# Kernel tuning notes

Hardware: AMD Instinct MI355X
Metric: run time of the kernel (lower is better)

## Reference

```python
import jax, jax.numpy as jnp
import numpy as np

D_IN = 1024
D_OUT = 1024

def setup_inputs() -> dict:
    key = jax.random.key(0)
    ks = jax.random.split(key, 7)
    s = 1.0 / np.sqrt(D_IN)
    x = jax.random.normal(ks[0], (4, 2048, D_IN), dtype=jnp.float32)
    Wq = jax.random.uniform(ks[1], (D_IN, D_OUT), jnp.float32, -s, s)
    Wk = jax.random.uniform(ks[2], (D_IN, D_OUT), jnp.float32, -s, s)
    Wv = jax.random.uniform(ks[3], (D_IN, D_OUT), jnp.float32, -s, s)
    bq = jax.random.uniform(ks[4], (D_OUT,), jnp.float32, -s, s)
    bk = jax.random.uniform(ks[5], (D_OUT,), jnp.float32, -s, s)
    bv = jax.random.uniform(ks[6], (D_OUT,), jnp.float32, -s, s)
    return {"x": x, "Wq": Wq, "Wk": Wk, "Wv": Wv, "bq": bq, "bk": bk, "bv": bv}

def reference(x, Wq, Wk, Wv, bq, bk, bv):
    # x: [b, n, d_in]
    q = jnp.einsum('bnd,de->bne', x, Wq) + bq
    k = jnp.einsum('bnd,de->bne', x, Wk) + bk
    v = jnp.einsum('bnd,de->bne', x, Wv) + bv
    scale = 1.0 / jnp.sqrt(jnp.asarray(k.shape[-1], dtype=x.dtype))
    scores = jnp.einsum('bqe,bke->bqk', q, k) * scale  # [b, n, n]
    weights = jax.nn.softmax(scores, axis=-1)
    return jnp.einsum('bqk,bke->bqe', weights, v)
```

## Files before the change

### kernel.cpp

```cpp
#include <hip/hip_runtime.h>
#include <cstdint>

typedef __bf16 bf16x8 __attribute__((ext_vector_type(8)));
typedef float f32x16 __attribute__((ext_vector_type(16)));

__device__ __forceinline__ unsigned short f2b(float f) {
    union { float f; uint32_t u; } x; x.f = f;
    uint32_t r = (x.u + 0x7fffu + ((x.u >> 16) & 1u)) >> 16;
    return (unsigned short)r;
}
__device__ __forceinline__ float b2f(unsigned short h) {
    union { float f; uint32_t u; } x; x.u = ((uint32_t)h) << 16;
    return x.f;
}

__global__ __launch_bounds__(256) void convert_x_kernel(const float* __restrict__ x,
                                                        unsigned short* __restrict__ xb) {
    int i = (blockIdx.x * 256 + threadIdx.x) * 4;
    float4 v = *(const float4*)(x + i);
    ushort4 o;
    o.x = f2b(v.x); o.y = f2b(v.y); o.z = f2b(v.z); o.w = f2b(v.w);
    *(ushort4*)(xb + i) = o;
}

__global__ __launch_bounds__(1024) void transpose_w_kernel(const float* __restrict__ Wq,
                                                           const float* __restrict__ Wk,
                                                           const float* __restrict__ Wv,
                                                           unsigned short* __restrict__ Wt) {
    __shared__ float tile[32][33];
    const float* W = (blockIdx.z == 0) ? Wq : (blockIdx.z == 1) ? Wk : Wv;
    int n0 = blockIdx.x * 32, k0 = blockIdx.y * 32;
    int tx = threadIdx.x, ty = threadIdx.y;
    tile[ty][tx] = W[(k0 + ty) * 1024 + n0 + tx];
    __syncthreads();
    Wt[((long)blockIdx.z * 1024 + n0 + ty) * 1024 + k0 + tx] = f2b(tile[tx][ty]);
}

template <int EPI>
__global__ __launch_bounds__(256) void gemm32(const unsigned short* __restrict__ A, int lda, long sA,
                                              const unsigned short* __restrict__ Bm, int ldb, long sB,
                                              void* __restrict__ Cv, long sC, int K,
                                              const float* __restrict__ bq, const float* __restrict__ bk,
                                              const float* __restrict__ bv,
                                              unsigned short* __restrict__ Qb,
                                              unsigned short* __restrict__ Kb,
                                              unsigned short* __restrict__ Vt) {
    __shared__ unsigned short As[128 * 64];
    __shared__ unsigned short Bs[128 * 64];

    const int tid = threadIdx.x;
    const int wave = tid >> 6, lane = tid & 63;
    const int h = lane >> 5;
    const int l31 = lane & 31;
    const int wm = wave >> 1, wn = wave & 1;
    const long bm = (long)blockIdx.y * 128;
    const long bn = (long)blockIdx.x * 128;

    const unsigned short* Ab = A + (long)blockIdx.z * sA;
    const unsigned short* Bb = Bm + (long)blockIdx.z * sB;

    f32x16 acc[2][2];
#pragma unroll
    for (int mi = 0; mi < 2; ++mi)
#pragma unroll
        for (int ni = 0; ni < 2; ++ni)
#pragma unroll
            for (int r = 0; r < 16; ++r) acc[mi][ni][r] = 0.0f;

    const int srow_in = lane >> 3;
    const int cswz = (lane & 7) ^ srow_in;
    const unsigned short* aptr[4];
    const unsigned short* bptr[4];
    unsigned short* asl[4];
    unsigned short* bsl[4];
#pragma unroll
    for (int j = 0; j < 4; ++j) {
        const int row = j * 32 + wave * 8 + srow_in;
        aptr[j] = Ab + (bm + row) * (long)lda + cswz * 8;
        bptr[j] = Bb + (bn + row) * (long)ldb + cswz * 8;
        asl[j] = &As[(j * 32 + wave * 8) * 64];
        bsl[j] = &Bs[(j * 32 + wave * 8) * 64];
    }

    const int arow0 = (wm * 64 + l31) * 64;
    const int brow0 = (wn * 64 + l31) * 64;
    int sw[4];
#pragma unroll
    for (int kh = 0; kh < 4; ++kh)
        sw[kh] = (((2 * kh + h) ^ (lane & 7)) * 8);

    for (int k0 = 0; k0 < K; k0 += 64) {
#pragma unroll
        for (int j = 0; j < 4; ++j) {
            __builtin_amdgcn_global_load_lds((const __attribute__((address_space(1))) void*)(aptr[j] + k0),
                                             (__attribute__((address_space(3))) void*)asl[j], 16, 0, 0);
            __builtin_amdgcn_global_load_lds((const __attribute__((address_space(1))) void*)(bptr[j] + k0),
                                             (__attribute__((address_space(3))) void*)bsl[j], 16, 0, 0);
        }
        __syncthreads();

#pragma unroll
        for (int kp = 0; kp < 2; ++kp) {
            bf16x8 af[2][2], bfr[2][2];
#pragma unroll
            for (int mi = 0; mi < 2; ++mi)
#pragma unroll
                for (int kk = 0; kk < 2; ++kk)
                    af[mi][kk] = *(const bf16x8*)&As[arow0 + mi * 32 * 64 + sw[kp * 2 + kk]];
#pragma unroll
            for (int ni = 0; ni < 2; ++ni)
#pragma unroll
                for (int kk = 0; kk < 2; ++kk)
                    bfr[ni][kk] = *(const bf16x8*)&Bs[brow0 + ni * 32 * 64 + sw[kp * 2 + kk]];
#pragma unroll
            for (int kk = 0; kk < 2; ++kk)
#pragma unroll
                for (int mi = 0; mi < 2; ++mi)
#pragma unroll
                    for (int ni = 0; ni < 2; ++ni)
                        acc[mi][ni] = __builtin_amdgcn_mfma_f32_32x32x16_bf16(af[mi][kk], bfr[ni][kk],
                                                                              acc[mi][ni], 0, 0, 0);
        }
        __syncthreads();
    }

#pragma unroll
    for (int mi = 0; mi < 2; ++mi) {
#pragma unroll
        for (int ni = 0; ni < 2; ++ni) {
            const f32x16 a = acc[mi][ni];
            const long col = bn + wn * 64 + ni * 32 + l31;
            const long rowB = bm + wm * 64 + mi * 32 + h * 4;
            if constexpr (EPI == 0) {
                if (col < 1024) {
                    const float bias = bq[col];
#pragma unroll
                    for (int g = 0; g < 4; ++g)
#pragma unroll
                        for (int r = 0; r < 4; ++r)
                            Qb[(rowB + g * 8 + r) * 1024 + col] = f2b((a[g * 4 + r] + bias) * 0.03125f);
                } else if (col < 2048) {
                    const float bias = bk[col - 1024];
#pragma unroll
                    for (int g = 0; g < 4; ++g)
#pragma unroll
                        for (int r = 0; r < 4; ++r)
                            Kb[(rowB + g * 8 + r) * 1024 + (col - 1024)] = f2b(a[g * 4 + r] + bias);
                } else {
                    const float bias = bv[col - 2048];
#pragma unroll
                    for (int g = 0; g < 4; ++g) {
                        const long row0 = rowB + g * 8;
                        const long batch = row0 >> 11;
                        const int n = (int)(row0 & 2047);
                        ushort4 o;
                        o.x = f2b(a[g * 4 + 0] + bias);
                        o.y = f2b(a[g * 4 + 1] + bias);
                        o.z = f2b(a[g * 4 + 2] + bias);
                        o.w = f2b(a[g * 4 + 3] + bias);
                        *(ushort4*)&Vt[(batch * 1024 + (col - 2048)) * 2048 + n] = o;
                    }
                }
            } else if constexpr (EPI == 1) {
                unsigned short* S = (unsigned short*)Cv + (long)blockIdx.z * sC;
#pragma unroll
                for (int g = 0; g < 4; ++g)
#pragma unroll
                    for (int r = 0; r < 4; ++r)
                        S[(rowB + g * 8 + r) * 2048 + col] = f2b(a[g * 4 + r]);
            } else {
                float* O = (float*)Cv + (long)blockIdx.z * sC;
#pragma unroll
                for (int g = 0; g < 4; ++g)
#pragma unroll
                    for (int r = 0; r < 4; ++r)
                        O[(rowB + g * 8 + r) * 1024 + col] = a[g * 4 + r];
            }
        }
    }
}

__global__ __launch_bounds__(256) void softmax_kernel(unsigned short* __restrict__ S) {
    const long row = blockIdx.x;
    unsigned short* p = S + row * 2048;
    const int tid = threadIdx.x;
    const int wave = tid >> 6, lane = tid & 63;

    ushort4 u0 = *(const ushort4*)&p[tid * 8];
    ushort4 u1 = *(const ushort4*)&p[tid * 8 + 4];
    float v[8];
    v[0] = b2f(u0.x); v[1] = b2f(u0.y); v[2] = b2f(u0.z); v[3] = b2f(u0.w);
    v[4] = b2f(u1.x); v[5] = b2f(u1.y); v[6] = b2f(u1.z); v[7] = b2f(u1.w);

    float m = v[0];
#pragma unroll
    for (int j = 1; j < 8; ++j) m = fmaxf(m, v[j]);
#pragma unroll
    for (int off = 32; off; off >>= 1) m = fmaxf(m, __shfl_xor(m, off, 64));
    __shared__ float redm[4];
    __shared__ float reds[4];
    if (lane == 0) redm[wave] = m;
    __syncthreads();
    m = fmaxf(fmaxf(redm[0], redm[1]), fmaxf(redm[2], redm[3]));

    float s = 0.0f;
#pragma unroll
    for (int j = 0; j < 8; ++j) { v[j] = __expf(v[j] - m); s += v[j]; }
#pragma unroll
    for (int off = 32; off; off >>= 1) s += __shfl_xor(s, off, 64);
    if (lane == 0) reds[wave] = s;
    __syncthreads();
    s = reds[0] + reds[1] + reds[2] + reds[3];
    const float inv = 1.0f / s;

    u0.x = f2b(v[0] * inv); u0.y = f2b(v[1] * inv); u0.z = f2b(v[2] * inv); u0.w = f2b(v[3] * inv);
    u1.x = f2b(v[4] * inv); u1.y = f2b(v[5] * inv); u1.z = f2b(v[6] * inv); u1.w = f2b(v[7] * inv);
    *(ushort4*)&p[tid * 8] = u0;
    *(ushort4*)&p[tid * 8 + 4] = u1;
}

extern "C" void kernel_launch(void* const* d_in, const int* in_sizes, int n_in,
                              void* d_out, int out_size, void* d_ws, size_t ws_size,
                              hipStream_t stream) {
    const float* x  = (const float*)d_in[0];
    const float* Wq = (const float*)d_in[1];
    const float* Wk = (const float*)d_in[2];
    const float* Wv = (const float*)d_in[3];
    const float* bq = (const float*)d_in[4];
    const float* bk = (const float*)d_in[5];
    const float* bv = (const float*)d_in[6];
    float* out = (float*)d_out;

    char* ws = (char*)d_ws;
    unsigned short* xb = (unsigned short*)ws; ws += 8192L * 1024 * 2;
    unsigned short* Wt = (unsigned short*)ws; ws += 3072L * 1024 * 2;
    unsigned short* Qb = (unsigned short*)ws; ws += 8192L * 1024 * 2;
    unsigned short* Kb = (unsigned short*)ws; ws += 8192L * 1024 * 2;
    unsigned short* Vt = (unsigned short*)ws; ws += 4L * 1024 * 2048 * 2;
    unsigned short* S  = (unsigned short*)ws; ws += 4L * 2048 * 2048 * 2;

    convert_x_kernel<<<8192, 256, 0, stream>>>(x, xb);
    transpose_w_kernel<<<dim3(32, 32, 3), dim3(32, 32), 0, stream>>>(Wq, Wk, Wv, Wt);
    gemm32<0><<<dim3(24, 64, 1), 256, 0, stream>>>(xb, 1024, 0, Wt, 1024, 0,
                                                   nullptr, 0, 1024, bq, bk, bv, Qb, Kb, Vt);
    gemm32<1><<<dim3(16, 16, 4), 256, 0, stream>>>(Qb, 1024, 2048L * 1024, Kb, 1024, 2048L * 1024,
                                                   S, 2048L * 2048, 1024,
                                                   nullptr, nullptr, nullptr, nullptr, nullptr, nullptr);
    softmax_kernel<<<8192, 256, 0, stream>>>(S);
    gemm32<2><<<dim3(8, 16, 4), 256, 0, stream>>>(S, 2048, 2048L * 2048, Vt, 2048, 2048L * 1024,
                                                  out, 2048L * 1024, 2048,
                                                  nullptr, nullptr, nullptr, nullptr, nullptr, nullptr);
}
```

Measured before the change: 279.9 us.

## Store B operands in MFMA fragment layout and load directly to registers

Weights, K and V are now written in a pre-swizzled fragment-major layout, so each lane's MFMA B operand is one contiguous 16-byte global load that bypasses LDS. Only the A tile still goes through LDS, which is now double-buffered so the next tile's load overlaps the MFMAs. This cuts LDS traffic and one barrier stage per iteration. In exchange, B reads from global or L2 are less shared across waves, and the K/V epilogue stores become scattered 2-byte writes.

```diff
diff --git a/kernel.cpp b/kernel.cpp
--- a/kernel.cpp
+++ b/kernel.cpp
@@ -12,6 +12,10 @@
 __device__ __forceinline__ float b2f(unsigned short h) {
     union { float f; uint32_t u; } x; x.u = ((uint32_t)h) << 16;
     return x.f;
+}
+
+__device__ __forceinline__ long foff(int n, int k, int K) {
+    return ((long)(n >> 5) * (K >> 4) + (k >> 4)) * 512 + (((k >> 3) & 1) * 32 + (n & 31)) * 8 + (k & 7);
 }
 
 __global__ __launch_bounds__(256) void convert_x_kernel(const float* __restrict__ x,
@@ -26,27 +30,28 @@
 __global__ __launch_bounds__(1024) void transpose_w_kernel(const float* __restrict__ Wq,
                                                            const float* __restrict__ Wk,
                                                            const float* __restrict__ Wv,
-                                                           unsigned short* __restrict__ Wt) {
+                                                           unsigned short* __restrict__ Wf) {
     __shared__ float tile[32][33];
     const float* W = (blockIdx.z == 0) ? Wq : (blockIdx.z == 1) ? Wk : Wv;
     int n0 = blockIdx.x * 32, k0 = blockIdx.y * 32;
     int tx = threadIdx.x, ty = threadIdx.y;
     tile[ty][tx] = W[(k0 + ty) * 1024 + n0 + tx];
     __syncthreads();
-    Wt[((long)blockIdx.z * 1024 + n0 + ty) * 1024 + k0 + tx] = f2b(tile[tx][ty]);
+    int n = blockIdx.z * 1024 + n0 + ty;
+    int k = k0 + tx;
+    Wf[foff(n, k, 1024)] = f2b(tile[tx][ty]);
 }
 
 template <int EPI>
-__global__ __launch_bounds__(256) void gemm32(const unsigned short* __restrict__ A, int lda, long sA,
-                                              const unsigned short* __restrict__ Bm, int ldb, long sB,
-                                              void* __restrict__ Cv, long sC, int K,
-                                              const float* __restrict__ bq, const float* __restrict__ bk,
-                                              const float* __restrict__ bv,
-                                              unsigned short* __restrict__ Qb,
-                                              unsigned short* __restrict__ Kb,
-                                              unsigned short* __restrict__ Vt) {
-    __shared__ unsigned short As[128 * 64];
-    __shared__ unsigned short Bs[128 * 64];
+__global__ __launch_bounds__(256) void gemm_fs(const unsigned short* __restrict__ A, int lda, long sA,
+                                               const unsigned short* __restrict__ Bf, long sB,
+                                               void* __restrict__ Cv, long sC, int K,
+                                               const float* __restrict__ bq, const float* __restrict__ bk,
+                                               const float* __restrict__ bv,
+                                               unsigned short* __restrict__ Qb,
+                                               unsigned short* __restrict__ Kf,
+                                               unsigned short* __restrict__ Vf) {
+    __shared__ unsigned short As[2][128 * 64];
 
     const int tid = threadIdx.x;
     const int wave = tid >> 6, lane = tid & 63;
@@ -57,7 +62,7 @@
     const long bn = (long)blockIdx.x * 128;
 
     const unsigned short* Ab = A + (long)blockIdx.z * sA;
-    const unsigned short* Bb = Bm + (long)blockIdx.z * sB;
+    const unsigned short* Bb = Bf + (long)blockIdx.z * sB;
 
     f32x16 acc[2][2];
 #pragma unroll
@@ -70,56 +75,62 @@
     const int srow_in = lane >> 3;
     const int cswz = (lane & 7) ^ srow_in;
     const unsigned short* aptr[4];
-    const unsigned short* bptr[4];
-    unsigned short* asl[4];
-    unsigned short* bsl[4];
+    int asloff[4];
 #pragma unroll
     for (int j = 0; j < 4; ++j) {
         const int row = j * 32 + wave * 8 + srow_in;
         aptr[j] = Ab + (bm + row) * (long)lda + cswz * 8;
-        bptr[j] = Bb + (bn + row) * (long)ldb + cswz * 8;
-        asl[j] = &As[(j * 32 + wave * 8) * 64];
-        bsl[j] = &Bs[(j * 32 + wave * 8) * 64];
-    }
-
-    const int arow0 = (wm * 64 + l31) * 64;
-    const int brow0 = (wn * 64 + l31) * 64;
-    int sw[4];
-#pragma unroll
-    for (int kh = 0; kh < 4; ++kh)
-        sw[kh] = (((2 * kh + h) ^ (lane & 7)) * 8);
-
-    for (int k0 = 0; k0 < K; k0 += 64) {
-#pragma unroll
-        for (int j = 0; j < 4; ++j) {
-            __builtin_amdgcn_global_load_lds((const __attribute__((address_space(1))) void*)(aptr[j] + k0),
-                                             (__attribute__((address_space(3))) void*)asl[j], 16, 0, 0);
-            __builtin_amdgcn_global_load_lds((const __attribute__((address_space(1))) void*)(bptr[j] + k0),
-                                             (__attribute__((address_space(3))) void*)bsl[j], 16, 0, 0);
+        asloff[j] = (j * 32 + wave * 8) * 64;
+    }
+
+    const unsigned short* bptr[2];
+#pragma unroll
+    for (int ni = 0; ni < 2; ++ni) {
+        const long nblk = (bn >> 5) + wn * 2 + ni;
+        bptr[ni] = Bb + nblk * (long)(K >> 4) * 512 + lane * 8;
+    }
+
+    int aoff[2][4];
+#pragma unroll
+    for (int mi = 0; mi < 2; ++mi)
+#pragma unroll
+        for (int kp = 0; kp < 4; ++kp)
+            aoff[mi][kp] = (wm * 64 + mi * 32 + l31) * 64 + (((kp * 2 + h) ^ (l31 & 7)) * 8);
+
+    const int nIter = K >> 6;
+
+#pragma unroll
+    for (int j = 0; j < 4; ++j)
+        __builtin_amdgcn_global_load_lds((const __attribute__((address_space(1))) void*)(aptr[j]),
+                                         (__attribute__((address_space(3))) void*)&As[0][asloff[j]], 16, 0, 0);
+    __syncthreads();
+
+    for (int it = 0; it < nIter; ++it) {
+        const int buf = it & 1;
+        if (it + 1 < nIter) {
+            const int koff = (it + 1) << 6;
+#pragma unroll
+            for (int j = 0; j < 4; ++j)
+                __builtin_amdgcn_global_load_lds((const __attribute__((address_space(1))) void*)(aptr[j] + koff),
+                                                 (__attribute__((address_space(3))) void*)&As[buf ^ 1][asloff[j]], 16, 0, 0);
         }
-        __syncthreads();
-
-#pragma unroll
-        for (int kp = 0; kp < 2; ++kp) {
-            bf16x8 af[2][2], bfr[2][2];
+        bf16x8 bfr[4][2];
+#pragma unroll
+        for (int kp = 0; kp < 4; ++kp)
+#pragma unroll
+            for (int ni = 0; ni < 2; ++ni)
+                bfr[kp][ni] = *(const bf16x8*)(bptr[ni] + (long)(it * 4 + kp) * 512);
+#pragma unroll
+        for (int kp = 0; kp < 4; ++kp) {
+            bf16x8 af[2];
 #pragma unroll
             for (int mi = 0; mi < 2; ++mi)
-#pragma unroll
-                for (int kk = 0; kk < 2; ++kk)
-                    af[mi][kk] = *(const bf16x8*)&As[arow0 + mi * 32 * 64 + sw[kp * 2 + kk]];
-#pragma unroll
-            for (int ni = 0; ni < 2; ++ni)
-#pragma unroll
-                for (int kk = 0; kk < 2; ++kk)
-                    bfr[ni][kk] = *(const bf16x8*)&Bs[brow0 + ni * 32 * 64 + sw[kp * 2 + kk]];
-#pragma unroll
-            for (int kk = 0; kk < 2; ++kk)
-#pragma unroll
-                for (int mi = 0; mi < 2; ++mi)
-#pragma unroll
-                    for (int ni = 0; ni < 2; ++ni)
-                        acc[mi][ni] = __builtin_amdgcn_mfma_f32_32x32x16_bf16(af[mi][kk], bfr[ni][kk],
-                                                                              acc[mi][ni], 0, 0, 0);
+                af[mi] = *(const bf16x8*)&As[buf][aoff[mi][kp]];
+#pragma unroll
+            for (int mi = 0; mi < 2; ++mi)
+#pragma unroll
+                for (int ni = 0; ni < 2; ++ni)
+                    acc[mi][ni] = __builtin_amdgcn_mfma_f32_32x32x16_bf16(af[mi], bfr[kp][ni], acc[mi][ni], 0, 0, 0);
         }
         __syncthreads();
     }
@@ -140,26 +151,33 @@
                         for (int r = 0; r < 4; ++r)
                             Qb[(rowB + g * 8 + r) * 1024 + col] = f2b((a[g * 4 + r] + bias) * 0.03125f);
                 } else if (col < 2048) {
-                    const float bias = bk[col - 1024];
+                    const int e = (int)col - 1024;
+                    const float bias = bk[e];
+                    const long batch = rowB >> 11;
+                    const int tokB = (int)(rowB & 2047) & ~31;
+                    unsigned short* dst = Kf + batch * (2048L * 1024) +
+                                          ((long)(tokB >> 5) * 64 + (e >> 4)) * 512 +
+                                          (long)(((e >> 3) & 1) * 32) * 8 + (e & 7);
 #pragma unroll
                     for (int g = 0; g < 4; ++g)
 #pragma unroll
-                        for (int r = 0; r < 4; ++r)
-                            Kb[(rowB + g * 8 + r) * 1024 + (col - 1024)] = f2b(a[g * 4 + r] + bias);
+                        for (int r = 0; r < 4; ++r) {
+                            const int tok31 = (int)((rowB + g * 8 + r) & 31);
+                            dst[tok31 * 8] = f2b(a[g * 4 + r] + bias);
+                        }
                 } else {
-                    const float bias = bv[col - 2048];
-#pragma unroll
-                    for (int g = 0; g < 4; ++g) {
-                        const long row0 = rowB + g * 8;
-                        const long batch = row0 >> 11;
-                        const int n = (int)(row0 & 2047);
-                        ushort4 o;
-                        o.x = f2b(a[g * 4 + 0] + bias);
-                        o.y = f2b(a[g * 4 + 1] + bias);
-                        o.z = f2b(a[g * 4 + 2] + bias);
-                        o.w = f2b(a[g * 4 + 3] + bias);
-                        *(ushort4*)&Vt[(batch * 1024 + (col - 2048)) * 2048 + n] = o;
-                    }
+                    const int e = (int)col - 2048;
+                    const float bias = bv[e];
+                    const long batch = rowB >> 11;
+                    unsigned short* base = Vf + batch * (2048L * 1024) + (long)(e >> 5) * 128 * 512 + l31 * 8;
+#pragma unroll
+                    for (int g = 0; g < 4; ++g)
+#pragma unroll
+                        for (int r = 0; r < 4; ++r) {
+                            const int tok = (int)((rowB + g * 8 + r) & 2047);
+                            base[((long)(tok >> 4)) * 512 + (long)(((tok >> 3) & 1) * 32) * 8 + (tok & 7)] =
+                                f2b(a[g * 4 + r] + bias);
+                        }
                 }
             } else if constexpr (EPI == 1) {
                 unsigned short* S = (unsigned short*)Cv + (long)blockIdx.z * sC;
@@ -233,21 +251,21 @@
 
     char* ws = (char*)d_ws;
     unsigned short* xb = (unsigned short*)ws; ws += 8192L * 1024 * 2;
-    unsigned short* Wt = (unsigned short*)ws; ws += 3072L * 1024 * 2;
+    unsigned short* Wf = (unsigned short*)ws; ws += 3072L * 1024 * 2;
     unsigned short* Qb = (unsigned short*)ws; ws += 8192L * 1024 * 2;
-    unsigned short* Kb = (unsigned short*)ws; ws += 8192L * 1024 * 2;
-    unsigned short* Vt = (unsigned short*)ws; ws += 4L * 1024 * 2048 * 2;
+    unsigned short* Kf = (unsigned short*)ws; ws += 8192L * 1024 * 2;
+    unsigned short* Vf = (unsigned short*)ws; ws += 8192L * 1024 * 2;
     unsigned short* S  = (unsigned short*)ws; ws += 4L * 2048 * 2048 * 2;
 
     convert_x_kernel<<<8192, 256, 0, stream>>>(x, xb);
-    transpose_w_kernel<<<dim3(32, 32, 3), dim3(32, 32), 0, stream>>>(Wq, Wk, Wv, Wt);
-    gemm32<0><<<dim3(24, 64, 1), 256, 0, stream>>>(xb, 1024, 0, Wt, 1024, 0,
-                                                   nullptr, 0, 1024, bq, bk, bv, Qb, Kb, Vt);
-    gemm32<1><<<dim3(16, 16, 4), 256, 0, stream>>>(Qb, 1024, 2048L * 1024, Kb, 1024, 2048L * 1024,
-                                                   S, 2048L * 2048, 1024,
+    transpose_w_kernel<<<dim3(32, 32, 3), dim3(32, 32), 0, stream>>>(Wq, Wk, Wv, Wf);
+    gemm_fs<0><<<dim3(24, 64, 1), 256, 0, stream>>>(xb, 1024, 0, Wf, 0,
+                                                    nullptr, 0, 1024, bq, bk, bv, Qb, Kf, Vf);
+    gemm_fs<1><<<dim3(16, 16, 4), 256, 0, stream>>>(Qb, 1024, 2048L * 1024, Kf, 2048L * 1024,
+                                                    S, 2048L * 2048, 1024,
+                                                    nullptr, nullptr, nullptr, nullptr, nullptr, nullptr);
+    softmax_kernel<<<8192, 256, 0, stream>>>(S);
+    gemm_fs<2><<<dim3(8, 16, 4), 256, 0, stream>>>(S, 2048, 2048L * 2048, Vf, 2048L * 1024,
+                                                   out, 2048L * 1024, 2048,
                                                    nullptr, nullptr, nullptr, nullptr, nullptr, nullptr);
-    softmax_kernel<<<8192, 256, 0, stream>>>(S);
-    gemm32<2><<<dim3(8, 16, 4), 256, 0, stream>>>(S, 2048, 2048L * 2048, Vt, 2048, 2048L * 1024,
-                                                  out, 2048L * 1024, 2048,
-                                                  nullptr, nullptr, nullptr, nullptr, nullptr, nullptr);
-}
+}
```

Result: no change. 283.9 us (+1.4%).
